# Kernel optimization log

Hardware: AMD Instinct MI355X
Metric: run time of the kernel (lower is better)

The kernel has to match this reference:

```python
import jax, jax.numpy as jnp
import numpy as np

B, T, D, H, L, F = 128, 512, 32, 128, 3, 4


def setup_inputs() -> dict:
    key = jax.random.key(0)
    ks = jax.random.split(key, 13)
    s = 0.05
    inp = {
        "x": jax.random.normal(ks[0], (B, T, D), dtype=jnp.float32),
        # layer 0 input weights [4H, D]; layers 1..L-1 input weights [L-1, 4H, H]
        "w_ih0": jax.random.normal(ks[1], (4 * H, D), dtype=jnp.float32) * s,
        "w_ih_rest": jax.random.normal(ks[2], (L - 1, 4 * H, H), dtype=jnp.float32) * s,
        "w_hh": jax.random.normal(ks[3], (L, 4 * H, H), dtype=jnp.float32) * s,
        "b_ih": jax.random.normal(ks[4], (L, 4 * H), dtype=jnp.float32) * s,
        "b_hh": jax.random.normal(ks[5], (L, 4 * H), dtype=jnp.float32) * s,
        "w_attn": jax.random.normal(ks[6], (1, H), dtype=jnp.float32) * s,
        "b_attn": jax.random.normal(ks[7], (1,), dtype=jnp.float32) * s,
        "w1": jax.random.normal(ks[8], (64, H), dtype=jnp.float32) * s,
        "b1": jax.random.normal(ks[9], (64,), dtype=jnp.float32) * s,
        "w2": jax.random.normal(ks[10], (F, 64), dtype=jnp.float32) * s,
        "b2": jax.random.normal(ks[11], (F,), dtype=jnp.float32) * s,
    }
    return inp


def _lstm_layer(xs, w_ih, w_hh, bi, bh):
    # xs: [B, T, Din] -> hs: [B, T, H]; PyTorch gate order i, f, g, o
    b, t = xs.shape[0], xs.shape[1]
    h_dim = w_hh.shape[1]
    pre = jnp.einsum('bti,gi->btg', xs, w_ih) + bi + bh  # [B, T, 4H]

    def step(carry, p_t):
        h, c = carry
        g = p_t + h @ w_hh.T
        i, f, gg, o = jnp.split(g, 4, axis=-1)
        i = jax.nn.sigmoid(i)
        f = jax.nn.sigmoid(f)
        gg = jnp.tanh(gg)
        o = jax.nn.sigmoid(o)
        c = f * c + i * gg
        h = o * jnp.tanh(c)
        return (h, c), h

    h0 = jnp.zeros((b, h_dim), xs.dtype)
    _, hs = jax.lax.scan(step, (h0, h0), jnp.swapaxes(pre, 0, 1))
    return jnp.swapaxes(hs, 0, 1)


def reference(x, w_ih0, w_ih_rest, w_hh, b_ih, b_hh, w_attn, b_attn, w1, b1, w2, b2):
    out = _lstm_layer(x, w_ih0, w_hh[0], b_ih[0], b_hh[0])
    for l in range(1, L):
        out = _lstm_layer(out, w_ih_rest[l - 1], w_hh[l], b_ih[l], b_hh[l])
    # additive attention pooling over time
    attn_w = jax.nn.softmax(jnp.einsum('bth,oh->bto', out, w_attn) + b_attn, axis=1)  # [B,T,1]
    ctx = jnp.sum(attn_w * out, axis=1)  # [B, H]
    # MLP head (dropout is identity at inference)
    h1 = jax.nn.relu(ctx @ w1.T + b1)
    return h1 @ w2.T + b2
```

## Files before the change

kernel.cpp:

```cpp
#include <hip/hip_runtime.h>
#include <math.h>

#define Bn 128
#define Tn 512
#define Dn 32
#define Hn 128
#define Gn 512
#define Ln 3

#define BAR_LDS() asm volatile("s_waitcnt lgkmcnt(0)\n\ts_barrier" ::: "memory")

typedef _Float16 h2 __attribute__((ext_vector_type(2)));
typedef _Float16 h4 __attribute__((ext_vector_type(4)));
typedef _Float16 half8 __attribute__((ext_vector_type(8)));
typedef float f32x4 __attribute__((ext_vector_type(4)));

__device__ __forceinline__ float dot2(h2 a, h2 b, float c) {
    return __builtin_amdgcn_fdot2(a, b, c, false);
}
__device__ __forceinline__ h2 pkh(float a, float b) {
    h2 r; r.x = (_Float16)a; r.y = (_Float16)b; return r;
}
__device__ __forceinline__ float sigm(float x) {
    return __builtin_amdgcn_rcpf(1.f + __expf(-x));
}
__device__ __forceinline__ float tanh_fast(float x) {
    return 1.f - 2.f * __builtin_amdgcn_rcpf(1.f + __expf(2.f * x));
}

#define DPPADD(a, CTRL) { \
    int _t = __builtin_amdgcn_update_dpp(0, __builtin_bit_cast(int, a), \
                                         CTRL, 0xF, 0xF, true); \
    a += __builtin_bit_cast(float, _t); }

#define KEEPH(x) asm volatile("" : "+v"(x))
#define LD8H(p) (*(const half8*)(p))
#define H2OF(V, i) (((const h2*)&(V))[i])

#define DECL16(P, R) \
  h2 P##0=pkh((R)[0],(R)[1]),   P##1=pkh((R)[2],(R)[3]),   P##2=pkh((R)[4],(R)[5]),   P##3=pkh((R)[6],(R)[7]),   \
     P##4=pkh((R)[8],(R)[9]),   P##5=pkh((R)[10],(R)[11]), P##6=pkh((R)[12],(R)[13]), P##7=pkh((R)[14],(R)[15]), \
     P##8=pkh((R)[16],(R)[17]), P##9=pkh((R)[18],(R)[19]), P##10=pkh((R)[20],(R)[21]),P##11=pkh((R)[22],(R)[23]),\
     P##12=pkh((R)[24],(R)[25]),P##13=pkh((R)[26],(R)[27]),P##14=pkh((R)[28],(R)[29]),P##15=pkh((R)[30],(R)[31]);
#define KEEP16(P) \
  KEEPH(P##0); KEEPH(P##1); KEEPH(P##2); KEEPH(P##3); KEEPH(P##4); KEEPH(P##5); \
  KEEPH(P##6); KEEPH(P##7); KEEPH(P##8); KEEPH(P##9); KEEPH(P##10); KEEPH(P##11); \
  KEEPH(P##12); KEEPH(P##13); KEEPH(P##14); KEEPH(P##15);

#define EXTRACT16(P, A, B, C, D) \
  h2 P##0 = H2OF(A,0), P##1 = H2OF(A,1), P##2  = H2OF(A,2), P##3  = H2OF(A,3), \
     P##4 = H2OF(B,0), P##5 = H2OF(B,1), P##6  = H2OF(B,2), P##7  = H2OF(B,3), \
     P##8 = H2OF(C,0), P##9 = H2OF(C,1), P##10 = H2OF(C,2), P##11 = H2OF(C,3), \
     P##12= H2OF(D,0), P##13= H2OF(D,1), P##14 = H2OF(D,2), P##15 = H2OF(D,3);

#define DOTA(j) { \
    aI = dot2(hvA##j, wiA##j, aI);  aF = dot2(hvA##j, wfA##j, aF); \
    aG = dot2(hvA##j, wgA##j, aG);  aO = dot2(hvA##j, woA##j, aO); }
#define DOTB(j) { \
    aI = dot2(hvB##j, wiB##j, aI);  aF = dot2(hvB##j, wfB##j, aF); \
    aG = dot2(hvB##j, wgB##j, aG);  aO = dot2(hvB##j, woB##j, aO); }
#define DOT4V(j) { \
    aI = dot2(hv##j, wi##j, aI);  aF = dot2(hv##j, wf##j, aF); \
    aG = dot2(hv##j, wg##j, aG);  aO = dot2(hv##j, wo##j, aO); }
#define DOT4Y(j) { \
    aI = dot2(pv##j, yi##j, aI);  aF = dot2(pv##j, yf##j, aF); \
    aG = dot2(pv##j, yg##j, aG);  aO = dot2(pv##j, yo##j, aO); }

template<typename TA>
__global__ __launch_bounds__(256) void gemm_pre(
    const TA* __restrict__ A, int K, int rowStrideB, int t0, int tlog,
    const float* __restrict__ W,
    const float* __restrict__ bi, const float* __restrict__ bh,
    _Float16* __restrict__ C)
{
    __shared__ h2 As2[64][20];
    __shared__ h2 Bs2[64][20];
    const int tid  = threadIdx.x;
    const int row0 = blockIdx.x * 64;
    const int col0 = blockIdx.y * 64;
    const int w    = tid >> 6;
    const int lane = tid & 63;
    const int qm   = (w >> 1) * 32;
    const int qn   = (w & 1) * 32;
    const int fm   = lane & 15;
    const int fq   = lane >> 4;
    const int tmask = (1 << tlog) - 1;
    const int lrow = tid >> 2;
    const int lk   = (tid & 3) * 8;

    f32x4 acc00 = {0,0,0,0}, acc01 = {0,0,0,0};
    f32x4 acc10 = {0,0,0,0}, acc11 = {0,0,0,0};

    for (int k0 = 0; k0 < K; k0 += 32) {
        {
            int rg = row0 + lrow;
            int b_idx = rg >> tlog, tt = rg & tmask;
            const TA* ap = A + (size_t)b_idx * rowStrideB +
                           (size_t)(t0 + tt) * K + (k0 + lk);
            if constexpr (sizeof(TA) == 2) {
                *(float4*)&As2[lrow][(tid & 3) * 4] = *(const float4*)ap;
            } else {
                float4 va = *(const float4*)ap;
                float4 vb = *(const float4*)(ap + 4);
                float4 o;
                ((h2*)&o)[0] = pkh(va.x, va.y);
                ((h2*)&o)[1] = pkh(va.z, va.w);
                ((h2*)&o)[2] = pkh(vb.x, vb.y);
                ((h2*)&o)[3] = pkh(vb.z, vb.w);
                *(float4*)&As2[lrow][(tid & 3) * 4] = o;
            }
            const float* wp = W + (size_t)(col0 + lrow) * K + (k0 + lk);
            float4 wa = *(const float4*)wp;
            float4 wb = *(const float4*)(wp + 4);
            float4 ow;
            ((h2*)&ow)[0] = pkh(wa.x, wa.y);
            ((h2*)&ow)[1] = pkh(wa.z, wa.w);
            ((h2*)&ow)[2] = pkh(wb.x, wb.y);
            ((h2*)&ow)[3] = pkh(wb.z, wb.w);
            *(float4*)&Bs2[lrow][(tid & 3) * 4] = ow;
        }
        __syncthreads();
        half8 a0 = *(const half8*)&As2[qm + fm][fq * 4];
        half8 a1 = *(const half8*)&As2[qm + 16 + fm][fq * 4];
        half8 b0 = *(const half8*)&Bs2[qn + fm][fq * 4];
        half8 b1 = *(const half8*)&Bs2[qn + 16 + fm][fq * 4];
        acc00 = __builtin_amdgcn_mfma_f32_16x16x32_f16(a0, b0, acc00, 0, 0, 0);
        acc01 = __builtin_amdgcn_mfma_f32_16x16x32_f16(a0, b1, acc01, 0, 0, 0);
        acc10 = __builtin_amdgcn_mfma_f32_16x16x32_f16(a1, b0, acc10, 0, 0, 0);
        acc11 = __builtin_amdgcn_mfma_f32_16x16x32_f16(a1, b1, acc11, 0, 0, 0);
        __syncthreads();
    }

    const int g0 = col0 + qn + fm;
    const int g1 = g0 + 16;
    const float bb0 = bi[g0] + bh[g0];
    const float bb1 = bi[g1] + bh[g1];
    const int m0 = row0 + qm + fq * 4;
    #pragma unroll
    for (int r = 0; r < 4; r++) {
        int ma = m0 + r, mb = m0 + 16 + r;
        C[((size_t)(ma >> 2) * Gn + g0) * 4 + (ma & 3)] = (_Float16)(acc00[r] + bb0);
        C[((size_t)(ma >> 2) * Gn + g1) * 4 + (ma & 3)] = (_Float16)(acc01[r] + bb1);
        C[((size_t)(mb >> 2) * Gn + g0) * 4 + (mb & 3)] = (_Float16)(acc10[r] + bb0);
        C[((size_t)(mb >> 2) * Gn + g1) * 4 + (mb & 3)] = (_Float16)(acc11[r] + bb1);
    }
}

__global__ __launch_bounds__(512)
__attribute__((amdgpu_waves_per_eu(2)))
void pipe(
    const _Float16* __restrict__ pre0,
    const float* __restrict__ w_hh,
    const float* __restrict__ wih1,
    const float* __restrict__ b_ih, const float* __restrict__ b_hh,
    _Float16* __restrict__ hs0,
    _Float16* __restrict__ hs1,
    int* __restrict__ flags)
{
    const int b    = blockIdx.x;
    const int layer= blockIdx.y;
    const int tid  = threadIdx.x;
    const int lane = tid & 63;
    const int wv   = tid >> 6;
    const int kq4  = lane & 3;
    const int u    = wv * 16 + (lane >> 2);

    __shared__ h2 hb[2][Hn / 2];
    __shared__ _Float16 hstage[2][16][Hn];
    __shared__ _Float16 pL[2][16][Hn];
    __shared__ float lds_pad[20480];

    if (pre0 == nullptr) {
        lds_pad[tid] = (float)tid;
        __syncthreads();
        ((float*)hs0)[tid] = lds_pad[(tid * 7) & 20479];
    }

    const float* whl = w_hh + (size_t)layer * Gn * Hn;
    const float* rI = whl + (size_t)(0 * Hn + u) * Hn + kq4 * 32;
    const float* rF = whl + (size_t)(1 * Hn + u) * Hn + kq4 * 32;
    const float* rG = whl + (size_t)(2 * Hn + u) * Hn + kq4 * 32;
    const float* rO = whl + (size_t)(3 * Hn + u) * Hn + kq4 * 32;
    DECL16(wi, rI) DECL16(wf, rF) DECL16(wg, rG) DECL16(wo, rO)
    KEEP16(wi) KEEP16(wf) KEEP16(wg) KEEP16(wo)

    if (tid < Hn / 2) hb[0][tid] = pkh(0.f, 0.f);

    float cr = 0.f;

    if (layer == 0) {
        __syncthreads();
        const float mI = (kq4 == 0) ? 1.f : 0.f;
        const float mF = (kq4 == 1) ? 1.f : 0.f;
        const float mG = (kq4 == 2) ? 1.f : 0.f;
        const float mO = (kq4 == 3) ? 1.f : 0.f;

        const h4* qq = (const h4*)pre0 + (size_t)(b * 128) * Gn + kq4 * Hn + u;
        _Float16* hs0b = hs0 + (size_t)b * Tn * Hn;

        h4 q0 = qq[0];
        h4 q1 = qq[Gn];
        const h4* pld = qq + 2 * (size_t)Gn;

        auto tick = [&](int t, float pv) {
            const h2* hrow = &hb[t & 1][kq4 * 16];
            half8 hA = LD8H(hrow);     half8 hB = LD8H(hrow + 4);
            half8 hC = LD8H(hrow + 8); half8 hD = LD8H(hrow + 12);
            EXTRACT16(hv, hA, hB, hC, hD)

            float aI = 0.f, aF = 0.f, aG = 0.f, aO = 0.f;
            DOT4V(0)  DOT4V(1)  DOT4V(2)  DOT4V(3)
            DOT4V(4)  DOT4V(5)  DOT4V(6)  DOT4V(7)
            DOT4V(8)  DOT4V(9)  DOT4V(10) DOT4V(11)
            DOT4V(12) DOT4V(13) DOT4V(14) DOT4V(15)

            aI = fmaf(pv, mI, aI);
            aF = fmaf(pv, mF, aF);
            aG = fmaf(pv, mG, aG);
            aO = fmaf(pv, mO, aO);

            DPPADD(aI, 0xB1) DPPADD(aF, 0xB1) DPPADD(aG, 0xB1) DPPADD(aO, 0xB1)
            DPPADD(aI, 0x4E) DPPADD(aF, 0x4E) DPPADD(aG, 0x4E) DPPADD(aO, 0x4E)

            float iv = sigm(aI);
            float fv = sigm(aF);
            float gv = tanh_fast(aG);
            float ov = sigm(aO);
            cr = fv * cr + iv * gv;
            float hnew = ov * tanh_fast(cr);
            _Float16 hh = (_Float16)hnew;
            if (kq4 == 0) {
                ((_Float16*)hb[(t + 1) & 1])[u] = hh;
                hstage[(t >> 4) & 1][t & 15][u] = hh;
            }
            BAR_LDS();
        };

        auto flush_pub = [&](int ch) {
            if (tid < 256) {
                float4 v = ((const float4*)&hstage[ch & 1][0][0])[tid];
                *(float4*)(hs0b + (size_t)ch * 16 * Hn + tid * 8) = v;
            }
            asm volatile("s_waitcnt vmcnt(0)" ::: "memory");
            __syncthreads();
            if (tid == 0)
                __hip_atomic_store(flags + b, ch + 1, __ATOMIC_RELEASE,
                                   __HIP_MEMORY_SCOPE_AGENT);
        };

        for (int qr = 0; qr < 126; qr++) {
            tick(4 * qr,     (float)q0.x);
            tick(4 * qr + 1, (float)q0.y);
            tick(4 * qr + 2, (float)q0.z);
            tick(4 * qr + 3, (float)q0.w);
            if ((qr & 3) == 3) flush_pub(qr >> 2);
            q0 = q1;
            q1 = *pld; pld += Gn;
        }
        tick(504, (float)q0.x); tick(505, (float)q0.y);
        tick(506, (float)q0.z); tick(507, (float)q0.w);
        q0 = q1;
        tick(508, (float)q0.x); tick(509, (float)q0.y);
        tick(510, (float)q0.z); tick(511, (float)q0.w);
        flush_pub(31);
    } else {
        const float* yIr = wih1 + (size_t)(0 * Hn + u) * Hn + kq4 * 32;
        const float* yFr = wih1 + (size_t)(1 * Hn + u) * Hn + kq4 * 32;
        const float* yGr = wih1 + (size_t)(2 * Hn + u) * Hn + kq4 * 32;
        const float* yOr = wih1 + (size_t)(3 * Hn + u) * Hn + kq4 * 32;
        DECL16(yi, yIr) DECL16(yf, yFr) DECL16(yg, yGr) DECL16(yo, yOr)
        KEEP16(yi) KEEP16(yf) KEEP16(yg) KEEP16(yo)

        const float bI1 = b_ih[Gn + 0 * Hn + u] + b_hh[Gn + 0 * Hn + u];
        const float bF1 = b_ih[Gn + 1 * Hn + u] + b_hh[Gn + 1 * Hn + u];
        const float bG1 = b_ih[Gn + 2 * Hn + u] + b_hh[Gn + 2 * Hn + u];
        const float bO1 = b_ih[Gn + 3 * Hn + u] + b_hh[Gn + 3 * Hn + u];

        const _Float16* hs0b = hs0 + (size_t)b * Tn * Hn;
        _Float16* hs1b = hs1 + (size_t)b * Tn * Hn;

        int avail = 0;
        auto gate = [&](int need) {
            if (avail >= need) return;
            do {
                int a0 = 0;
                if (lane == 0)
                    a0 = __hip_atomic_load(flags + b, __ATOMIC_ACQUIRE,
                                           __HIP_MEMORY_SCOPE_AGENT);
                avail = __builtin_amdgcn_readfirstlane(a0);
                if (avail < need) __builtin_amdgcn_s_sleep(8);
            } while (avail < need);
        };

        auto tick = [&](int t) {
            const h2* h1row = &hb[t & 1][kq4 * 16];
            half8 hA = LD8H(h1row);     half8 hB = LD8H(h1row + 4);
            half8 hC = LD8H(h1row + 8); half8 hD = LD8H(h1row + 12);
            EXTRACT16(hv, hA, hB, hC, hD)
            const h2* h0row = (const h2*)&pL[(t >> 4) & 1][t & 15][kq4 * 32];
            half8 pA = LD8H(h0row);     half8 pB = LD8H(h0row + 4);
            half8 pC = LD8H(h0row + 8); half8 pD = LD8H(h0row + 12);
            EXTRACT16(pv, pA, pB, pC, pD)

            float aI = 0.f, aF = 0.f, aG = 0.f, aO = 0.f;
            DOT4V(0)  DOT4V(1)  DOT4V(2)  DOT4V(3)
            DOT4V(4)  DOT4V(5)  DOT4V(6)  DOT4V(7)
            DOT4V(8)  DOT4V(9)  DOT4V(10) DOT4V(11)
            DOT4V(12) DOT4V(13) DOT4V(14) DOT4V(15)
            DOT4Y(0)  DOT4Y(1)  DOT4Y(2)  DOT4Y(3)
            DOT4Y(4)  DOT4Y(5)  DOT4Y(6)  DOT4Y(7)
            DOT4Y(8)  DOT4Y(9)  DOT4Y(10) DOT4Y(11)
            DOT4Y(12) DOT4Y(13) DOT4Y(14) DOT4Y(15)

            DPPADD(aI, 0xB1) DPPADD(aF, 0xB1) DPPADD(aG, 0xB1) DPPADD(aO, 0xB1)
            DPPADD(aI, 0x4E) DPPADD(aF, 0x4E) DPPADD(aG, 0x4E) DPPADD(aO, 0x4E)

            float iv = sigm(aI + bI1);
            float fv = sigm(aF + bF1);
            float gv = tanh_fast(aG + bG1);
            float ov = sigm(aO + bO1);
            cr = fv * cr + iv * gv;
            float hnew = ov * tanh_fast(cr);
            _Float16 hh = (_Float16)hnew;
            if (kq4 == 0) {
                ((_Float16*)hb[(t + 1) & 1])[u] = hh;
                hstage[(t >> 4) & 1][t & 15][u] = hh;
            }
            BAR_LDS();
        };

        gate(1);
        if (tid < 256) {
            float4 v = *(const float4*)(hs0b + tid * 8);
            *(float4*)((_Float16*)&pL[0][0][0] + tid * 8) = v;
        }
        __syncthreads();

        for (int c = 0; c < 32; c++) {
            if (c + 1 < 32) {
                gate(c + 2);
                if (tid < 256) {
                    float4 v = *(const float4*)(hs0b +
                                (size_t)(c + 1) * 16 * Hn + tid * 8);
                    *(float4*)((_Float16*)&pL[(c + 1) & 1][0][0] + tid * 8) = v;
                }
            }
            #pragma unroll
            for (int tt = 0; tt < 16; tt++) tick(16 * c + tt);
            if (tid < 256) {
                float4 v = ((const float4*)&hstage[c & 1][0][0])[tid];
                *(float4*)(hs1b + (size_t)c * 16 * Hn + tid * 8) = v;
            }
        }
    }
}

__global__ __launch_bounds__(256)
__attribute__((amdgpu_waves_per_eu(1, 2)))
void scan256(
    const _Float16* __restrict__ pre,
    const float* __restrict__ w_hh,
    _Float16* __restrict__ hs16)
{
    const int b    = blockIdx.x;
    const int tid  = threadIdx.x;
    const int lane = tid & 63;
    const int wv   = tid >> 6;
    const int kq   = lane & 1;
    const int u    = wv * 32 + (lane >> 1);

    __shared__ h2 hbuf[2][Hn / 2];
    __shared__ _Float16 hstage[2][16][Hn];
    __shared__ float lds_pad[19456];

    if (pre == nullptr) {
        lds_pad[tid] = (float)tid;
        __syncthreads();
        ((float*)hs16)[tid] = lds_pad[(tid * 7) & 19455];
    }

    const float* rI = w_hh + (size_t)(0 * Hn + u) * Hn + kq * 64;
    const float* rF = w_hh + (size_t)(1 * Hn + u) * Hn + kq * 64;
    const float* rG = w_hh + (size_t)(2 * Hn + u) * Hn + kq * 64;
    const float* rO = w_hh + (size_t)(3 * Hn + u) * Hn + kq * 64;
    DECL16(wiA, rI) DECL16(wiB, (rI + 32))
    DECL16(wfA, rF) DECL16(wfB, (rF + 32))
    DECL16(wgA, rG) DECL16(wgB, (rG + 32))
    DECL16(woA, rO) DECL16(woB, (rO + 32))
    KEEP16(wiA) KEEP16(wiB) KEEP16(wfA) KEEP16(wfB)
    KEEP16(wgA) KEEP16(wgB) KEEP16(woA) KEEP16(woB)

    if (tid < Hn / 2) hbuf[0][tid] = pkh(0.f, 0.f);
    __syncthreads();

    const h4* qq = (const h4*)pre + (size_t)(b * 128) * Gn + u;
    _Float16* hsb = hs16 + (size_t)b * Tn * Hn;

    const float ms = (kq == 0) ? 1.f : 0.f;

    h4 qI0 = qq[0],   qF0 = qq[128],      qG0 = qq[256],      qO0 = qq[384];
    h4 qI1 = qq[Gn],  qF1 = qq[Gn + 128], qG1 = qq[Gn + 256], qO1 = qq[Gn + 384];
    const h4* pld = qq + 2 * (size_t)Gn;

    float cr = 0.f;

    auto body = [&](int t, float vI, float vF, float vG, float vO) {
        const h2* hrow = &hbuf[t & 1][kq * 32];
        half8 hA = LD8H(hrow);      half8 hB = LD8H(hrow + 4);
        half8 hC = LD8H(hrow + 8);  half8 hD = LD8H(hrow + 12);
        half8 hE = LD8H(hrow + 16); half8 hF_ = LD8H(hrow + 20);
        half8 hG_ = LD8H(hrow + 24); half8 hH_ = LD8H(hrow + 28);
        EXTRACT16(hvA, hA, hB, hC, hD)
        EXTRACT16(hvB, hE, hF_, hG_, hH_)

        float aI = vI, aF = vF, aG = vG, aO = vO;
        DOTA(0)  DOTA(1)  DOTA(2)  DOTA(3)
        DOTA(4)  DOTA(5)  DOTA(6)  DOTA(7)
        DOTA(8)  DOTA(9)  DOTA(10) DOTA(11)
        DOTA(12) DOTA(13) DOTA(14) DOTA(15)
        DOTB(0)  DOTB(1)  DOTB(2)  DOTB(3)
        DOTB(4)  DOTB(5)  DOTB(6)  DOTB(7)
        DOTB(8)  DOTB(9)  DOTB(10) DOTB(11)
        DOTB(12) DOTB(13) DOTB(14) DOTB(15)

        DPPADD(aI, 0xB1) DPPADD(aF, 0xB1) DPPADD(aG, 0xB1) DPPADD(aO, 0xB1)

        float iv = sigm(aI);
        float fv = sigm(aF);
        float gv = tanh_fast(aG);
        float ov = sigm(aO);
        cr = fv * cr + iv * gv;
        float hnew = ov * tanh_fast(cr);
        _Float16 hh = (_Float16)hnew;
        if (kq == 0) {
            ((_Float16*)hbuf[(t + 1) & 1])[u] = hh;
            hstage[(t >> 4) & 1][t & 15][u] = hh;
        }
        BAR_LDS();
    };

    auto flush = [&](int ch) {
        const float4* src = (const float4*)&hstage[ch & 1][0][0];
        float4 v = src[tid];
        *(float4*)(hsb + (size_t)ch * 16 * Hn + tid * 8) = v;
    };

    for (int qr = 0; qr < 126; qr++) {
        body(4 * qr,     ms * (float)qI0.x, ms * (float)qF0.x,
                         ms * (float)qG0.x, ms * (float)qO0.x);
        body(4 * qr + 1, ms * (float)qI0.y, ms * (float)qF0.y,
                         ms * (float)qG0.y, ms * (float)qO0.y);
        body(4 * qr + 2, ms * (float)qI0.z, ms * (float)qF0.z,
                         ms * (float)qG0.z, ms * (float)qO0.z);
        body(4 * qr + 3, ms * (float)qI0.w, ms * (float)qF0.w,
                         ms * (float)qG0.w, ms * (float)qO0.w);
        if ((qr & 3) == 3) flush(qr >> 2);
        qI0 = qI1; qF0 = qF1; qG0 = qG1; qO0 = qO1;
        qI1 = pld[0]; qF1 = pld[128]; qG1 = pld[256]; qO1 = pld[384];
        pld += Gn;
    }
    body(504, ms * (float)qI0.x, ms * (float)qF0.x,
              ms * (float)qG0.x, ms * (float)qO0.x);
    body(505, ms * (float)qI0.y, ms * (float)qF0.y,
              ms * (float)qG0.y, ms * (float)qO0.y);
    body(506, ms * (float)qI0.z, ms * (float)qF0.z,
              ms * (float)qG0.z, ms * (float)qO0.z);
    body(507, ms * (float)qI0.w, ms * (float)qF0.w,
              ms * (float)qG0.w, ms * (float)qO0.w);
    qI0 = qI1; qF0 = qF1; qG0 = qG1; qO0 = qO1;
    body(508, ms * (float)qI0.x, ms * (float)qF0.x,
              ms * (float)qG0.x, ms * (float)qO0.x);
    body(509, ms * (float)qI0.y, ms * (float)qF0.y,
              ms * (float)qG0.y, ms * (float)qO0.y);
    body(510, ms * (float)qI0.z, ms * (float)qF0.z,
              ms * (float)qG0.z, ms * (float)qO0.z);
    body(511, ms * (float)qI0.w, ms * (float)qF0.w,
              ms * (float)qG0.w, ms * (float)qO0.w);
    flush(31);
}

__global__ __launch_bounds__(256) void head_kernel(
    const _Float16* __restrict__ hs16,
    const float* __restrict__ w_attn, const float* __restrict__ b_attn,
    const float* __restrict__ w1, const float* __restrict__ b1,
    const float* __restrict__ w2, const float* __restrict__ b2,
    float* __restrict__ out)
{
    const int b = blockIdx.x;
    const int tid = threadIdx.x;
    __shared__ h2 wa2[Hn / 2];
    __shared__ __align__(16) float sc[Tn];
    __shared__ __align__(16) float red[256];
    __shared__ __align__(16) float ctx_sh[Hn];
    __shared__ __align__(16) float h1_sh[64];

    if (tid < Hn / 2) wa2[tid] = pkh(w_attn[2 * tid], w_attn[2 * tid + 1]);
    __syncthreads();

    const _Float16* hb = hs16 + (size_t)b * Tn * Hn;

    for (int t = tid; t < Tn; t += 256) {
        const h2* hp = (const h2*)(hb + (size_t)t * Hn);
        float s = 0.f;
        #pragma unroll
        for (int k = 0; k < 64; k++) s = dot2(hp[k], wa2[k], s);
        sc[t] = s + b_attn[0];
    }
    __syncthreads();

    float m = fmaxf(sc[tid], sc[tid + 256]);
    red[tid] = m; __syncthreads();
    for (int s_ = 128; s_ > 0; s_ >>= 1) {
        if (tid < s_) red[tid] = fmaxf(red[tid], red[tid + s_]);
        __syncthreads();
    }
    float mx = red[0];
    __syncthreads();
    float e0 = __expf(sc[tid] - mx), e1 = __expf(sc[tid + 256] - mx);
    sc[tid] = e0; sc[tid + 256] = e1;
    red[tid] = e0 + e1; __syncthreads();
    for (int s_ = 128; s_ > 0; s_ >>= 1) {
        if (tid < s_) red[tid] += red[tid + s_];
        __syncthreads();
    }
    float inv = 1.f / red[0];
    __syncthreads();

    {
        int jj = tid & 127, half = tid >> 7;
        float a = 0.f;
        for (int t = half * 256; t < half * 256 + 256; t++)
            a += sc[t] * (float)hb[(size_t)t * Hn + jj];
        red[tid] = a;
        __syncthreads();
        if (tid < Hn) ctx_sh[tid] = (red[tid] + red[tid + Hn]) * inv;
        __syncthreads();
    }

    if (tid < 64) {
        const float4* wvv = (const float4*)(w1 + (size_t)tid * Hn);
        const float4* cv = (const float4*)ctx_sh;
        float s = 0.f;
        #pragma unroll
        for (int k = 0; k < 32; k++) {
            float4 a = wvv[k], c = cv[k];
            s += a.x * c.x + a.y * c.y + a.z * c.z + a.w * c.w;
        }
        h1_sh[tid] = fmaxf(s + b1[tid], 0.f);
    }
    __syncthreads();

    if (tid < 4) {
        float s = 0.f;
        const float* wvv = w2 + tid * 64;
        #pragma unroll
        for (int k = 0; k < 64; k++) s += wvv[k] * h1_sh[k];
        out[b * 4 + tid] = s + b2[tid];
    }
}

extern "C" void kernel_launch(void* const* d_in, const int* in_sizes, int n_in,
                              void* d_out, int out_size, void* d_ws, size_t ws_size,
                              hipStream_t stream)
{
    const float* x        = (const float*)d_in[0];
    const float* w_ih0    = (const float*)d_in[1];
    const float* w_ih_rest= (const float*)d_in[2];
    const float* w_hh     = (const float*)d_in[3];
    const float* b_ih     = (const float*)d_in[4];
    const float* b_hh     = (const float*)d_in[5];
    const float* w_attn   = (const float*)d_in[6];
    const float* b_attn   = (const float*)d_in[7];
    const float* w1       = (const float*)d_in[8];
    const float* b1       = (const float*)d_in[9];
    const float* w2       = (const float*)d_in[10];
    const float* b2       = (const float*)d_in[11];
    float* out = (float*)d_out;

    const size_t nHS  = (size_t)Bn * Tn * Hn;
    const size_t nPRE = (size_t)Bn * Tn * Gn;

    _Float16* preh = (_Float16*)d_ws;
    _Float16* hs0  = preh + nPRE;
    _Float16* hs1  = hs0 + nHS;
    _Float16* hs2  = hs1 + nHS;
    int* flags     = (int*)(hs2 + nHS);

    hipMemsetAsync(flags, 0, Bn * sizeof(int), stream);

    gemm_pre<float><<<dim3(Bn * Tn / 64, 8), 256, 0, stream>>>(
        x, Dn, Tn * Dn, 0, 9, w_ih0, b_ih, b_hh, preh);

    pipe<<<dim3(Bn, 2), 512, 0, stream>>>(preh, w_hh, w_ih_rest,
                                          b_ih, b_hh, hs0, hs1, flags);

    gemm_pre<_Float16><<<dim3(Bn * Tn / 64, 8), 256, 0, stream>>>(
        hs1, Hn, Tn * Hn, 0, 9, w_ih_rest + (size_t)Gn * Hn,
        b_ih + 2 * Gn, b_hh + 2 * Gn, preh);
    scan256<<<Bn, 256, 0, stream>>>(preh, w_hh + 2 * (size_t)Gn * Hn, hs2);

    head_kernel<<<Bn, 256, 0, stream>>>(hs2, w_attn, b_attn, w1, b1, w2, b2, out);
}
```

Measured before the change: 894.0 us.

## Pipeline layer 2 into the wavefront kernel, reusing layer-0 blocks as consumers

Removes the separate layer-2 input GEMM and scan256 kernel. The layer-0 blocks, once their own recurrence finishes, run layer 2 as a flag-gated consumer of layer 1's output. Layer 1 now publishes per-chunk flags that layer 2 waits on. This lets layer 2 overlap with the tail of layer 1 and cuts kernel launches and the preactivation round trip. The cost is that layer 2 also performs the input projection inside its recurrent step, adding dot products on the critical path.

```diff
diff --git a/kernel.cpp b/kernel.cpp
--- a/kernel.cpp
+++ b/kernel.cpp
@@ -53,12 +53,6 @@
      P##8 = H2OF(C,0), P##9 = H2OF(C,1), P##10 = H2OF(C,2), P##11 = H2OF(C,3), \
      P##12= H2OF(D,0), P##13= H2OF(D,1), P##14 = H2OF(D,2), P##15 = H2OF(D,3);
 
-#define DOTA(j) { \
-    aI = dot2(hvA##j, wiA##j, aI);  aF = dot2(hvA##j, wfA##j, aF); \
-    aG = dot2(hvA##j, wgA##j, aG);  aO = dot2(hvA##j, woA##j, aO); }
-#define DOTB(j) { \
-    aI = dot2(hvB##j, wiB##j, aI);  aF = dot2(hvB##j, wfB##j, aF); \
-    aG = dot2(hvB##j, wgB##j, aG);  aO = dot2(hvB##j, woB##j, aO); }
 #define DOT4V(j) { \
     aI = dot2(hv##j, wi##j, aI);  aF = dot2(hv##j, wf##j, aF); \
     aG = dot2(hv##j, wg##j, aG);  aO = dot2(hv##j, wo##j, aO); }
@@ -146,19 +140,136 @@
     }
 }
 
+__device__ __forceinline__ void consumer_phase(
+    int b, int tid, int lane, int kq4, int u,
+    const _Float16* __restrict__ hsin_b,
+    _Float16* __restrict__ hsout_b,
+    const float* __restrict__ whh,
+    const float* __restrict__ wih,
+    const float* __restrict__ bih, const float* __restrict__ bhh,
+    int* __restrict__ gate_flags,
+    int* __restrict__ pub_flags,
+    h2* hb_, _Float16* hst_, _Float16* pL_)
+{
+    const float* rI = whh + (size_t)(0 * Hn + u) * Hn + kq4 * 32;
+    const float* rF = whh + (size_t)(1 * Hn + u) * Hn + kq4 * 32;
+    const float* rG = whh + (size_t)(2 * Hn + u) * Hn + kq4 * 32;
+    const float* rO = whh + (size_t)(3 * Hn + u) * Hn + kq4 * 32;
+    DECL16(wi, rI) DECL16(wf, rF) DECL16(wg, rG) DECL16(wo, rO)
+    KEEP16(wi) KEEP16(wf) KEEP16(wg) KEEP16(wo)
+
+    const float* yIr = wih + (size_t)(0 * Hn + u) * Hn + kq4 * 32;
+    const float* yFr = wih + (size_t)(1 * Hn + u) * Hn + kq4 * 32;
+    const float* yGr = wih + (size_t)(2 * Hn + u) * Hn + kq4 * 32;
+    const float* yOr = wih + (size_t)(3 * Hn + u) * Hn + kq4 * 32;
+    DECL16(yi, yIr) DECL16(yf, yFr) DECL16(yg, yGr) DECL16(yo, yOr)
+    KEEP16(yi) KEEP16(yf) KEEP16(yg) KEEP16(yo)
+
+    const float bI1 = bih[0 * Hn + u] + bhh[0 * Hn + u];
+    const float bF1 = bih[1 * Hn + u] + bhh[1 * Hn + u];
+    const float bG1 = bih[2 * Hn + u] + bhh[2 * Hn + u];
+    const float bO1 = bih[3 * Hn + u] + bhh[3 * Hn + u];
+
+    if (tid < Hn / 2) hb_[tid] = pkh(0.f, 0.f);
+    float cr = 0.f;
+
+    int avail = 0;
+    auto gate = [&](int need) {
+        if (avail >= need) return;
+        do {
+            int a0 = 0;
+            if (lane == 0)
+                a0 = __hip_atomic_load(gate_flags + b, __ATOMIC_ACQUIRE,
+                                       __HIP_MEMORY_SCOPE_AGENT);
+            avail = __builtin_amdgcn_readfirstlane(a0);
+            if (avail < need) __builtin_amdgcn_s_sleep(8);
+        } while (avail < need);
+    };
+
+    auto tick = [&](int t) {
+        const h2* h1row = hb_ + (t & 1) * (Hn / 2) + kq4 * 16;
+        half8 hA = LD8H(h1row);     half8 hB = LD8H(h1row + 4);
+        half8 hC = LD8H(h1row + 8); half8 hD = LD8H(h1row + 12);
+        EXTRACT16(hv, hA, hB, hC, hD)
+        const h2* h0row = (const h2*)(pL_ + ((t >> 4) & 1) * 2048 +
+                                      (t & 15) * Hn + kq4 * 32);
+        half8 pA = LD8H(h0row);     half8 pB = LD8H(h0row + 4);
+        half8 pC = LD8H(h0row + 8); half8 pD = LD8H(h0row + 12);
+        EXTRACT16(pv, pA, pB, pC, pD)
+
+        float aI = 0.f, aF = 0.f, aG = 0.f, aO = 0.f;
+        DOT4V(0)  DOT4V(1)  DOT4V(2)  DOT4V(3)
+        DOT4V(4)  DOT4V(5)  DOT4V(6)  DOT4V(7)
+        DOT4V(8)  DOT4V(9)  DOT4V(10) DOT4V(11)
+        DOT4V(12) DOT4V(13) DOT4V(14) DOT4V(15)
+        DOT4Y(0)  DOT4Y(1)  DOT4Y(2)  DOT4Y(3)
+        DOT4Y(4)  DOT4Y(5)  DOT4Y(6)  DOT4Y(7)
+        DOT4Y(8)  DOT4Y(9)  DOT4Y(10) DOT4Y(11)
+        DOT4Y(12) DOT4Y(13) DOT4Y(14) DOT4Y(15)
+
+        DPPADD(aI, 0xB1) DPPADD(aF, 0xB1) DPPADD(aG, 0xB1) DPPADD(aO, 0xB1)
+        DPPADD(aI, 0x4E) DPPADD(aF, 0x4E) DPPADD(aG, 0x4E) DPPADD(aO, 0x4E)
+
+        float iv = sigm(aI + bI1);
+        float fv = sigm(aF + bF1);
+        float gv = tanh_fast(aG + bG1);
+        float ov = sigm(aO + bO1);
+        cr = fv * cr + iv * gv;
+        float hnew = ov * tanh_fast(cr);
+        _Float16 hh = (_Float16)hnew;
+        if (kq4 == 0) {
+            ((_Float16*)(hb_ + ((t + 1) & 1) * (Hn / 2)))[u] = hh;
+            hst_[((t >> 4) & 1) * 2048 + (t & 15) * Hn + u] = hh;
+        }
+        BAR_LDS();
+    };
+
+    gate(1);
+    if (tid < 256) {
+        float4 v = *(const float4*)(hsin_b + tid * 8);
+        *(float4*)(pL_ + tid * 8) = v;
+    }
+    __syncthreads();
+
+    for (int c = 0; c < 32; c++) {
+        if (c + 1 < 32) {
+            gate(c + 2);
+            if (tid < 256) {
+                float4 v = *(const float4*)(hsin_b +
+                            (size_t)(c + 1) * 16 * Hn + tid * 8);
+                *(float4*)(pL_ + ((c + 1) & 1) * 2048 + tid * 8) = v;
+            }
+        }
+        #pragma unroll
+        for (int tt = 0; tt < 16; tt++) tick(16 * c + tt);
+        if (tid < 256) {
+            float4 v = ((const float4*)(hst_ + (c & 1) * 2048))[tid];
+            *(float4*)(hsout_b + (size_t)c * 16 * Hn + tid * 8) = v;
+        }
+        if (pub_flags != nullptr) {
+            asm volatile("s_waitcnt vmcnt(0)" ::: "memory");
+            __syncthreads();
+            if (tid == 0)
+                __hip_atomic_store(pub_flags + b, c + 1, __ATOMIC_RELEASE,
+                                   __HIP_MEMORY_SCOPE_AGENT);
+        }
+    }
+}
+
 __global__ __launch_bounds__(512)
 __attribute__((amdgpu_waves_per_eu(2)))
-void pipe(
+void pipe3(
     const _Float16* __restrict__ pre0,
     const float* __restrict__ w_hh,
-    const float* __restrict__ wih1,
+    const float* __restrict__ wih_rest,
     const float* __restrict__ b_ih, const float* __restrict__ b_hh,
     _Float16* __restrict__ hs0,
     _Float16* __restrict__ hs1,
-    int* __restrict__ flags)
+    _Float16* __restrict__ hs2,
+    int* __restrict__ flags0, int* __restrict__ flags1)
 {
     const int b    = blockIdx.x;
-    const int layer= blockIdx.y;
+    const int role = blockIdx.y;
     const int tid  = threadIdx.x;
     const int lane = tid & 63;
     const int wv   = tid >> 6;
@@ -176,20 +287,18 @@
         ((float*)hs0)[tid] = lds_pad[(tid * 7) & 20479];
     }
 
-    const float* whl = w_hh + (size_t)layer * Gn * Hn;
-    const float* rI = whl + (size_t)(0 * Hn + u) * Hn + kq4 * 32;
-    const float* rF = whl + (size_t)(1 * Hn + u) * Hn + kq4 * 32;
-    const float* rG = whl + (size_t)(2 * Hn + u) * Hn + kq4 * 32;
-    const float* rO = whl + (size_t)(3 * Hn + u) * Hn + kq4 * 32;
-    DECL16(wi, rI) DECL16(wf, rF) DECL16(wg, rG) DECL16(wo, rO)
-    KEEP16(wi) KEEP16(wf) KEEP16(wg) KEEP16(wo)
-
-    if (tid < Hn / 2) hb[0][tid] = pkh(0.f, 0.f);
-
-    float cr = 0.f;
-
-    if (layer == 0) {
-        __syncthreads();
+    if (role == 0) {
+        const float* whl = w_hh;
+        const float* rI = whl + (size_t)(0 * Hn + u) * Hn + kq4 * 32;
+        const float* rF = whl + (size_t)(1 * Hn + u) * Hn + kq4 * 32;
+        const float* rG = whl + (size_t)(2 * Hn + u) * Hn + kq4 * 32;
+        const float* rO = whl + (size_t)(3 * Hn + u) * Hn + kq4 * 32;
+        DECL16(wi, rI) DECL16(wf, rF) DECL16(wg, rG) DECL16(wo, rO)
+        KEEP16(wi) KEEP16(wf) KEEP16(wg) KEEP16(wo)
+
+        if (tid < Hn / 2) hb[0][tid] = pkh(0.f, 0.f);
+        __syncthreads();
+
         const float mI = (kq4 == 0) ? 1.f : 0.f;
         const float mF = (kq4 == 1) ? 1.f : 0.f;
         const float mG = (kq4 == 2) ? 1.f : 0.f;
@@ -201,6 +310,8 @@
         h4 q0 = qq[0];
         h4 q1 = qq[Gn];
         const h4* pld = qq + 2 * (size_t)Gn;
+
+        float cr = 0.f;
 
         auto tick = [&](int t, float pv) {
             const h2* hrow = &hb[t & 1][kq4 * 16];
@@ -244,7 +355,7 @@
             asm volatile("s_waitcnt vmcnt(0)" ::: "memory");
             __syncthreads();
             if (tid == 0)
-                __hip_atomic_store(flags + b, ch + 1, __ATOMIC_RELEASE,
+                __hip_atomic_store(flags0 + b, ch + 1, __ATOMIC_RELEASE,
                                    __HIP_MEMORY_SCOPE_AGENT);
         };
 
@@ -263,220 +374,26 @@
         tick(508, (float)q0.x); tick(509, (float)q0.y);
         tick(510, (float)q0.z); tick(511, (float)q0.w);
         flush_pub(31);
+
+        __syncthreads();
+        consumer_phase(b, tid, lane, kq4, u,
+                       hs1 + (size_t)b * Tn * Hn,
+                       hs2 + (size_t)b * Tn * Hn,
+                       w_hh + 2 * (size_t)Gn * Hn,
+                       wih_rest + (size_t)Gn * Hn,
+                       b_ih + 2 * Gn, b_hh + 2 * Gn,
+                       flags1, nullptr,
+                       &hb[0][0], &hstage[0][0][0], &pL[0][0][0]);
     } else {
-        const float* yIr = wih1 + (size_t)(0 * Hn + u) * Hn + kq4 * 32;
-        const float* yFr = wih1 + (size_t)(1 * Hn + u) * Hn + kq4 * 32;
-        const float* yGr = wih1 + (size_t)(2 * Hn + u) * Hn + kq4 * 32;
-        const float* yOr = wih1 + (size_t)(3 * Hn + u) * Hn + kq4 * 32;
-        DECL16(yi, yIr) DECL16(yf, yFr) DECL16(yg, yGr) DECL16(yo, yOr)
-        KEEP16(yi) KEEP16(yf) KEEP16(yg) KEEP16(yo)
-
-        const float bI1 = b_ih[Gn + 0 * Hn + u] + b_hh[Gn + 0 * Hn + u];
-        const float bF1 = b_ih[Gn + 1 * Hn + u] + b_hh[Gn + 1 * Hn + u];
-        const float bG1 = b_ih[Gn + 2 * Hn + u] + b_hh[Gn + 2 * Hn + u];
-        const float bO1 = b_ih[Gn + 3 * Hn + u] + b_hh[Gn + 3 * Hn + u];
-
-        const _Float16* hs0b = hs0 + (size_t)b * Tn * Hn;
-        _Float16* hs1b = hs1 + (size_t)b * Tn * Hn;
-
-        int avail = 0;
-        auto gate = [&](int need) {
-            if (avail >= need) return;
-            do {
-                int a0 = 0;
-                if (lane == 0)
-                    a0 = __hip_atomic_load(flags + b, __ATOMIC_ACQUIRE,
-                                           __HIP_MEMORY_SCOPE_AGENT);
-                avail = __builtin_amdgcn_readfirstlane(a0);
-                if (avail < need) __builtin_amdgcn_s_sleep(8);
-            } while (avail < need);
-        };
-
-        auto tick = [&](int t) {
-            const h2* h1row = &hb[t & 1][kq4 * 16];
-            half8 hA = LD8H(h1row);     half8 hB = LD8H(h1row + 4);
-            half8 hC = LD8H(h1row + 8); half8 hD = LD8H(h1row + 12);
-            EXTRACT16(hv, hA, hB, hC, hD)
-            const h2* h0row = (const h2*)&pL[(t >> 4) & 1][t & 15][kq4 * 32];
-            half8 pA = LD8H(h0row);     half8 pB = LD8H(h0row + 4);
-            half8 pC = LD8H(h0row + 8); half8 pD = LD8H(h0row + 12);
-            EXTRACT16(pv, pA, pB, pC, pD)
-
-            float aI = 0.f, aF = 0.f, aG = 0.f, aO = 0.f;
-            DOT4V(0)  DOT4V(1)  DOT4V(2)  DOT4V(3)
-            DOT4V(4)  DOT4V(5)  DOT4V(6)  DOT4V(7)
-            DOT4V(8)  DOT4V(9)  DOT4V(10) DOT4V(11)
-            DOT4V(12) DOT4V(13) DOT4V(14) DOT4V(15)
-            DOT4Y(0)  DOT4Y(1)  DOT4Y(2)  DOT4Y(3)
-            DOT4Y(4)  DOT4Y(5)  DOT4Y(6)  DOT4Y(7)
-            DOT4Y(8)  DOT4Y(9)  DOT4Y(10) DOT4Y(11)
-            DOT4Y(12) DOT4Y(13) DOT4Y(14) DOT4Y(15)
-
-            DPPADD(aI, 0xB1) DPPADD(aF, 0xB1) DPPADD(aG, 0xB1) DPPADD(aO, 0xB1)
-            DPPADD(aI, 0x4E) DPPADD(aF, 0x4E) DPPADD(aG, 0x4E) DPPADD(aO, 0x4E)
-
-            float iv = sigm(aI + bI1);
-            float fv = sigm(aF + bF1);
-            float gv = tanh_fast(aG + bG1);
-            float ov = sigm(aO + bO1);
-            cr = fv * cr + iv * gv;
-            float hnew = ov * tanh_fast(cr);
-            _Float16 hh = (_Float16)hnew;
-            if (kq4 == 0) {
-                ((_Float16*)hb[(t + 1) & 1])[u] = hh;
-                hstage[(t >> 4) & 1][t & 15][u] = hh;
-            }
-            BAR_LDS();
-        };
-
-        gate(1);
-        if (tid < 256) {
-            float4 v = *(const float4*)(hs0b + tid * 8);
-            *(float4*)((_Float16*)&pL[0][0][0] + tid * 8) = v;
-        }
-        __syncthreads();
-
-        for (int c = 0; c < 32; c++) {
-            if (c + 1 < 32) {
-                gate(c + 2);
-                if (tid < 256) {
-                    float4 v = *(const float4*)(hs0b +
-                                (size_t)(c + 1) * 16 * Hn + tid * 8);
-                    *(float4*)((_Float16*)&pL[(c + 1) & 1][0][0] + tid * 8) = v;
-                }
-            }
-            #pragma unroll
-            for (int tt = 0; tt < 16; tt++) tick(16 * c + tt);
-            if (tid < 256) {
-                float4 v = ((const float4*)&hstage[c & 1][0][0])[tid];
-                *(float4*)(hs1b + (size_t)c * 16 * Hn + tid * 8) = v;
-            }
-        }
-    }
-}
-
-__global__ __launch_bounds__(256)
-__attribute__((amdgpu_waves_per_eu(1, 2)))
-void scan256(
-    const _Float16* __restrict__ pre,
-    const float* __restrict__ w_hh,
-    _Float16* __restrict__ hs16)
-{
-    const int b    = blockIdx.x;
-    const int tid  = threadIdx.x;
-    const int lane = tid & 63;
-    const int wv   = tid >> 6;
-    const int kq   = lane & 1;
-    const int u    = wv * 32 + (lane >> 1);
-
-    __shared__ h2 hbuf[2][Hn / 2];
-    __shared__ _Float16 hstage[2][16][Hn];
-    __shared__ float lds_pad[19456];
-
-    if (pre == nullptr) {
-        lds_pad[tid] = (float)tid;
-        __syncthreads();
-        ((float*)hs16)[tid] = lds_pad[(tid * 7) & 19455];
-    }
-
-    const float* rI = w_hh + (size_t)(0 * Hn + u) * Hn + kq * 64;
-    const float* rF = w_hh + (size_t)(1 * Hn + u) * Hn + kq * 64;
-    const float* rG = w_hh + (size_t)(2 * Hn + u) * Hn + kq * 64;
-    const float* rO = w_hh + (size_t)(3 * Hn + u) * Hn + kq * 64;
-    DECL16(wiA, rI) DECL16(wiB, (rI + 32))
-    DECL16(wfA, rF) DECL16(wfB, (rF + 32))
-    DECL16(wgA, rG) DECL16(wgB, (rG + 32))
-    DECL16(woA, rO) DECL16(woB, (rO + 32))
-    KEEP16(wiA) KEEP16(wiB) KEEP16(wfA) KEEP16(wfB)
-    KEEP16(wgA) KEEP16(wgB) KEEP16(woA) KEEP16(woB)
-
-    if (tid < Hn / 2) hbuf[0][tid] = pkh(0.f, 0.f);
-    __syncthreads();
-
-    const h4* qq = (const h4*)pre + (size_t)(b * 128) * Gn + u;
-    _Float16* hsb = hs16 + (size_t)b * Tn * Hn;
-
-    const float ms = (kq == 0) ? 1.f : 0.f;
-
-    h4 qI0 = qq[0],   qF0 = qq[128],      qG0 = qq[256],      qO0 = qq[384];
-    h4 qI1 = qq[Gn],  qF1 = qq[Gn + 128], qG1 = qq[Gn + 256], qO1 = qq[Gn + 384];
-    const h4* pld = qq + 2 * (size_t)Gn;
-
-    float cr = 0.f;
-
-    auto body = [&](int t, float vI, float vF, float vG, float vO) {
-        const h2* hrow = &hbuf[t & 1][kq * 32];
-        half8 hA = LD8H(hrow);      half8 hB = LD8H(hrow + 4);
-        half8 hC = LD8H(hrow + 8);  half8 hD = LD8H(hrow + 12);
-        half8 hE = LD8H(hrow + 16); half8 hF_ = LD8H(hrow + 20);
-        half8 hG_ = LD8H(hrow + 24); half8 hH_ = LD8H(hrow + 28);
-        EXTRACT16(hvA, hA, hB, hC, hD)
-        EXTRACT16(hvB, hE, hF_, hG_, hH_)
-
-        float aI = vI, aF = vF, aG = vG, aO = vO;
-        DOTA(0)  DOTA(1)  DOTA(2)  DOTA(3)
-        DOTA(4)  DOTA(5)  DOTA(6)  DOTA(7)
-        DOTA(8)  DOTA(9)  DOTA(10) DOTA(11)
-        DOTA(12) DOTA(13) DOTA(14) DOTA(15)
-        DOTB(0)  DOTB(1)  DOTB(2)  DOTB(3)
-        DOTB(4)  DOTB(5)  DOTB(6)  DOTB(7)
-        DOTB(8)  DOTB(9)  DOTB(10) DOTB(11)
-        DOTB(12) DOTB(13) DOTB(14) DOTB(15)
-
-        DPPADD(aI, 0xB1) DPPADD(aF, 0xB1) DPPADD(aG, 0xB1) DPPADD(aO, 0xB1)
-
-        float iv = sigm(aI);
-        float fv = sigm(aF);
-        float gv = tanh_fast(aG);
-        float ov = sigm(aO);
-        cr = fv * cr + iv * gv;
-        float hnew = ov * tanh_fast(cr);
-        _Float16 hh = (_Float16)hnew;
-        if (kq == 0) {
-            ((_Float16*)hbuf[(t + 1) & 1])[u] = hh;
-            hstage[(t >> 4) & 1][t & 15][u] = hh;
-        }
-        BAR_LDS();
-    };
-
-    auto flush = [&](int ch) {
-        const float4* src = (const float4*)&hstage[ch & 1][0][0];
-        float4 v = src[tid];
-        *(float4*)(hsb + (size_t)ch * 16 * Hn + tid * 8) = v;
-    };
-
-    for (int qr = 0; qr < 126; qr++) {
-        body(4 * qr,     ms * (float)qI0.x, ms * (float)qF0.x,
-                         ms * (float)qG0.x, ms * (float)qO0.x);
-        body(4 * qr + 1, ms * (float)qI0.y, ms * (float)qF0.y,
-                         ms * (float)qG0.y, ms * (float)qO0.y);
-        body(4 * qr + 2, ms * (float)qI0.z, ms * (float)qF0.z,
-                         ms * (float)qG0.z, ms * (float)qO0.z);
-        body(4 * qr + 3, ms * (float)qI0.w, ms * (float)qF0.w,
-                         ms * (float)qG0.w, ms * (float)qO0.w);
-        if ((qr & 3) == 3) flush(qr >> 2);
-        qI0 = qI1; qF0 = qF1; qG0 = qG1; qO0 = qO1;
-        qI1 = pld[0]; qF1 = pld[128]; qG1 = pld[256]; qO1 = pld[384];
-        pld += Gn;
-    }
-    body(504, ms * (float)qI0.x, ms * (float)qF0.x,
-              ms * (float)qG0.x, ms * (float)qO0.x);
-    body(505, ms * (float)qI0.y, ms * (float)qF0.y,
-              ms * (float)qG0.y, ms * (float)qO0.y);
-    body(506, ms * (float)qI0.z, ms * (float)qF0.z,
-              ms * (float)qG0.z, ms * (float)qO0.z);
-    body(507, ms * (float)qI0.w, ms * (float)qF0.w,
-              ms * (float)qG0.w, ms * (float)qO0.w);
-    qI0 = qI1; qF0 = qF1; qG0 = qG1; qO0 = qO1;
-    body(508, ms * (float)qI0.x, ms * (float)qF0.x,
-              ms * (float)qG0.x, ms * (float)qO0.x);
-    body(509, ms * (float)qI0.y, ms * (float)qF0.y,
-              ms * (float)qG0.y, ms * (float)qO0.y);
-    body(510, ms * (float)qI0.z, ms * (float)qF0.z,
-              ms * (float)qG0.z, ms * (float)qO0.z);
-    body(511, ms * (float)qI0.w, ms * (float)qF0.w,
-              ms * (float)qG0.w, ms * (float)qO0.w);
-    flush(31);
+        consumer_phase(b, tid, lane, kq4, u,
+                       hs0 + (size_t)b * Tn * Hn,
+                       hs1 + (size_t)b * Tn * Hn,
+                       w_hh + (size_t)Gn * Hn,
+                       wih_rest,
+                       b_ih + Gn, b_hh + Gn,
+                       flags0, flags1,
+                       &hb[0][0], &hstage[0][0][0], &pL[0][0][0]);
+    }
 }
 
 __global__ __launch_bounds__(256) void head_kernel(
@@ -584,20 +501,17 @@
     _Float16* hs0  = preh + nPRE;
     _Float16* hs1  = hs0 + nHS;
     _Float16* hs2  = hs1 + nHS;
-    int* flags     = (int*)(hs2 + nHS);
-
-    hipMemsetAsync(flags, 0, Bn * sizeof(int), stream);
+    int* flags0    = (int*)(hs2 + nHS);
+    int* flags1    = flags0 + Bn;
+
+    hipMemsetAsync(flags0, 0, 2 * Bn * sizeof(int), stream);
 
     gemm_pre<float><<<dim3(Bn * Tn / 64, 8), 256, 0, stream>>>(
         x, Dn, Tn * Dn, 0, 9, w_ih0, b_ih, b_hh, preh);
 
-    pipe<<<dim3(Bn, 2), 512, 0, stream>>>(preh, w_hh, w_ih_rest,
-                                          b_ih, b_hh, hs0, hs1, flags);
-
-    gemm_pre<_Float16><<<dim3(Bn * Tn / 64, 8), 256, 0, stream>>>(
-        hs1, Hn, Tn * Hn, 0, 9, w_ih_rest + (size_t)Gn * Hn,
-        b_ih + 2 * Gn, b_hh + 2 * Gn, preh);
-    scan256<<<Bn, 256, 0, stream>>>(preh, w_hh + 2 * (size_t)Gn * Hn, hs2);
+    pipe3<<<dim3(Bn, 2), 512, 0, stream>>>(preh, w_hh, w_ih_rest,
+                                           b_ih, b_hh, hs0, hs1, hs2,
+                                           flags0, flags1);
 
     head_kernel<<<Bn, 256, 0, stream>>>(hs2, w_attn, b_attn, w1, b1, w2, b2, out);
 }
```

Result: no change. 907.3 us (+1.5%).
